# Kernel optimization log

Hardware: AMD Instinct MI355X
Metric: run time of the kernel (lower is better)

## Reference

```python
import jax, jax.numpy as jnp
import numpy as np
import math

EMBED = 512
KDIM = 512
VDIM = 512
H = 8
HD = EMBED // H
N = 2048
L = 2048
B = 4


def setup_inputs() -> dict:
    key = jax.random.key(0)
    ks = jax.random.split(key, 14)
    s = 1.0 / math.sqrt(EMBED)
    return {
        "q": jax.random.normal(ks[0], (N, B, EMBED), jnp.float32),
        "k": jax.random.normal(ks[1], (L, B, KDIM), jnp.float32),
        "v": jax.random.normal(ks[2], (L, B, VDIM), jnp.float32),
        "pe1": jax.random.normal(ks[3], (B, N, 3), jnp.float32),
        "pe2": jax.random.normal(ks[4], (L, 3), jnp.float32),
        "Wq": jax.random.normal(ks[5], (EMBED, EMBED), jnp.float32) * s,
        "bq": jnp.zeros((EMBED,), jnp.float32),
        "Wk": jax.random.normal(ks[6], (EMBED, KDIM), jnp.float32) * s,
        "bk": jnp.zeros((EMBED,), jnp.float32),
        "Wv": jax.random.normal(ks[7], (EMBED, VDIM), jnp.float32) * s,
        "bv": jnp.zeros((EMBED,), jnp.float32),
        "Wo": jax.random.normal(ks[8], (EMBED, EMBED), jnp.float32) * s,
        "bo": jnp.zeros((EMBED,), jnp.float32),
    }


def reference(q, k, v, pe1, pe2, Wq, bq, Wk, bk, Wv, bv, Wo, bo):
    n, b, _ = q.shape
    l = k.shape[0]
    # projections (nn.Linear: x @ W.T + b)
    qp = q @ Wq.T + bq  # (n, b, E)
    kp = k @ Wk.T + bk  # (l, b, E)
    vp = v @ Wv.T + bv  # (l, b, E)
    # split heads -> (b, H, n, hd)
    qh = qp.reshape(n, b, H, HD).transpose(1, 2, 0, 3)
    kh = kp.reshape(l, b, H, HD).transpose(1, 2, 0, 3)
    vh = vp.reshape(l, b, H, HD).transpose(1, 2, 0, 3)
    # relative PE bias: (b, n, l), broadcast over heads
    pe_scores = jnp.einsum('bnc,lc->bnl', pe1, pe2)[:, None, :, :]
    scores = (jnp.einsum('bhnd,bhld->bhnl', qh, kh) + pe_scores) / math.sqrt(HD)
    attn = jax.nn.softmax(scores, axis=-1)
    out = jnp.einsum('bhnl,bhld->bhnd', attn, vh)  # (b, H, n, hd)
    out = out.transpose(2, 0, 1, 3).reshape(n, b, EMBED)
    return out @ Wo.T + bo
```

## Files before the change

kernel.cpp:

```cpp
#include <hip/hip_runtime.h>
#include <math.h>

#define EMBED 512
#define HDIM 64
#define NHEADS 8
#define SEQ_N 2048
#define SEQ_L 2048
#define BATCH 4
#define MROWS (SEQ_N*BATCH)
#define BE (BATCH*EMBED)

#define QSCALE 0.18033688f

typedef _Float16 f16;
typedef _Float16 half8 __attribute__((ext_vector_type(8)));
typedef _Float16 half4 __attribute__((ext_vector_type(4)));
typedef _Float16 half2v __attribute__((ext_vector_type(2)));
typedef float floatx4 __attribute__((ext_vector_type(4)));
typedef float floatx16 __attribute__((ext_vector_type(16)));

static __device__ inline float fast_exp2(float x) {
#if __has_builtin(__builtin_amdgcn_exp2f)
  return __builtin_amdgcn_exp2f(x);
#else
  return __expf(x * 0.69314718056f);
#endif
}

static __device__ inline half2v pk2(float a, float b) {
#if __has_builtin(__builtin_amdgcn_cvt_pkrtz)
  return __builtin_bit_cast(half2v, __builtin_amdgcn_cvt_pkrtz(a, b));
#else
  half2v o; o[0] = (f16)a; o[1] = (f16)b; return o;
#endif
}

static __device__ inline void gload16(const void* g, void* l) {
  __builtin_amdgcn_global_load_lds(
      (__attribute__((address_space(1))) void*)(g),
      (__attribute__((address_space(3))) void*)(l), 16, 0, 0);
}

__global__ __launch_bounds__(256) void cvt_all(const float* __restrict__ q,
                                               const float* __restrict__ k,
                                               const float* __restrict__ v,
                                               const float* __restrict__ Wq,
                                               const float* __restrict__ Wk,
                                               const float* __restrict__ Wv,
                                               const float* __restrict__ Wo,
                                               f16* __restrict__ qb, f16* __restrict__ kb,
                                               f16* __restrict__ vb, f16* __restrict__ Wb) {
  const long TOK = (long)MROWS * EMBED;
  const long WSZ = (long)EMBED * EMBED;
  int y = blockIdx.y;
  long i = ((long)blockIdx.x * 256 + threadIdx.x) * 4;
  if (y < 3) {
    if (i < TOK) {
      const float* s = y == 0 ? q : y == 1 ? k : v;
      f16* d = y == 0 ? qb : y == 1 ? kb : vb;
      float4 f = *reinterpret_cast<const float4*>(s + i);
      half4 o; o[0] = (f16)f.x; o[1] = (f16)f.y; o[2] = (f16)f.z; o[3] = (f16)f.w;
      *reinterpret_cast<half4*>(d + i) = o;
    }
  } else {
    if (i < 4 * WSZ) {
      int sel = (int)(i >> 18);
      long off = i & (WSZ - 1);
      const float* s = sel == 0 ? Wq : sel == 1 ? Wk : sel == 2 ? Wv : Wo;
      float4 f = *reinterpret_cast<const float4*>(s + off);
      half4 o; o[0] = (f16)f.x; o[1] = (f16)f.y; o[2] = (f16)f.z; o[3] = (f16)f.w;
      *reinterpret_cast<half4*>(Wb + i) = o;
    }
  }
}

__global__ __launch_bounds__(256) void gemm_qkv(const f16* __restrict__ A0,
                                                const f16* __restrict__ A1,
                                                const f16* __restrict__ A2,
                                                const f16* __restrict__ W0,
                                                const f16* __restrict__ W1,
                                                const f16* __restrict__ W2,
                                                const float* __restrict__ b0,
                                                const float* __restrict__ b1,
                                                const float* __restrict__ b2,
                                                f16* __restrict__ C0, f16* __restrict__ C1,
                                                f16* __restrict__ C2t) {
  __shared__ alignas(16) unsigned char gsm[34816];
  f16* As = reinterpret_cast<f16*>(gsm);
  f16* Bs = reinterpret_cast<f16*>(gsm + 16384);
  f16* T  = reinterpret_cast<f16*>(gsm);
  const int sel = blockIdx.y >> 2;
  const f16* A = sel == 0 ? A0 : sel == 1 ? A1 : A2;
  const f16* Bt = sel == 0 ? W0 : sel == 1 ? W1 : W2;
  const float* bias = sel == 0 ? b0 : sel == 1 ? b1 : b2;
  const float scl = sel == 0 ? QSCALE : 1.0f;
  const int tid = threadIdx.x;
  const int wave = tid >> 6, lane = tid & 63, quad = lane >> 4, l16 = lane & 15;
  const int wm = wave & 1, wn = wave >> 1;
  const long m0 = (long)blockIdx.x * 128;
  const long n0 = (long)(blockIdx.y & 3) * 128;
  const int srow = lane >> 2;
  const int scol = (lane & 3) * 8;

  const f16* Ag0 = A + (m0 + wave * 32 + srow) * EMBED + scol;
  const f16* Ag1 = A + (m0 + wave * 32 + 16 + srow) * EMBED + scol;
  const f16* Bg0 = Bt + (n0 + wave * 32 + srow) * EMBED + scol;
  const f16* Bg1 = Bt + (n0 + wave * 32 + 16 + srow) * EMBED + scol;

  gload16(Ag0, &As[(wave * 32) * 32]);
  gload16(Ag1, &As[(wave * 32 + 16) * 32]);
  gload16(Bg0, &Bs[(wave * 32) * 32]);
  gload16(Bg1, &Bs[(wave * 32 + 16) * 32]);
  floatx4 acc[4][4] = {};
  asm volatile("s_waitcnt vmcnt(0)" ::: "memory");
  __builtin_amdgcn_s_barrier();

#pragma unroll
  for (int ks = 0; ks < 16; ++ks) {
    const int cur = ks & 1;
    if (ks + 1 < 16) {
      const int k1 = (ks + 1) * 32;
      gload16(Ag0 + k1, &As[(cur ^ 1) * 4096 + (wave * 32) * 32]);
      gload16(Ag1 + k1, &As[(cur ^ 1) * 4096 + (wave * 32 + 16) * 32]);
      gload16(Bg0 + k1, &Bs[(cur ^ 1) * 4096 + (wave * 32) * 32]);
      gload16(Bg1 + k1, &Bs[(cur ^ 1) * 4096 + (wave * 32 + 16) * 32]);
    }
    half8 af[4], bf[4];
#pragma unroll
    for (int i = 0; i < 4; ++i)
      af[i] = *reinterpret_cast<const half8*>(&As[cur * 4096 + (wm * 64 + i * 16 + l16) * 32 + quad * 8]);
#pragma unroll
    for (int j = 0; j < 4; ++j)
      bf[j] = *reinterpret_cast<const half8*>(&Bs[cur * 4096 + (wn * 64 + j * 16 + l16) * 32 + quad * 8]);
#pragma unroll
    for (int i = 0; i < 4; ++i)
#pragma unroll
      for (int j = 0; j < 4; ++j)
        acc[i][j] = __builtin_amdgcn_mfma_f32_16x16x32_f16(af[i], bf[j], acc[i][j], 0, 0, 0);
    if (ks + 1 < 16) {
      asm volatile("s_waitcnt vmcnt(0)" ::: "memory");
      __builtin_amdgcn_s_barrier();
    }
  }

  if (sel != 2) {
    f16* C = sel == 0 ? C0 : C1;
#pragma unroll
    for (int i = 0; i < 4; ++i)
#pragma unroll
      for (int r = 0; r < 4; ++r) {
        long row = m0 + wm * 64 + i * 16 + quad * 4 + r;
#pragma unroll
        for (int j = 0; j < 4; ++j) {
          long col = n0 + wn * 64 + j * 16 + l16;
          float val = (acc[i][j][r] + bias[col]) * scl;
          C[row * EMBED + col] = (f16)val;
        }
      }
  } else {
    __syncthreads();
#pragma unroll
    for (int i = 0; i < 4; ++i)
#pragma unroll
      for (int r = 0; r < 4; ++r) {
        int mrow = wm * 64 + i * 16 + quad * 4 + r;
        int bq = mrow & 3, lt = mrow >> 2;
#pragma unroll
        for (int j = 0; j < 4; ++j) {
          int col = wn * 64 + j * 16 + l16;
          float val = acc[i][j][r] + bias[n0 + col];
          T[col * 136 + bq * 32 + lt] = (f16)val;
        }
      }
    __syncthreads();
    const int h0 = (int)(n0 >> 6);
    const long lbase = m0 >> 2;
#pragma unroll
    for (int it = 0; it < 8; ++it) {
      int f = it * 256 + tid;
      int ls = f & 3, bq = (f >> 2) & 3, d6 = (f >> 4) & 63, hl = f >> 10;
      half8 o = *reinterpret_cast<const half8*>(&T[(hl * 64 + d6) * 136 + bq * 32 + ls * 8]);
      *reinterpret_cast<half8*>(C2t + (((long)bq * 8 + h0 + hl) * 64 + d6) * 2048 + lbase + ls * 8) = o;
    }
  }
}

__global__ __launch_bounds__(256) void gemm_out(const f16* __restrict__ A,
                                                const f16* __restrict__ Bt,
                                                const float* __restrict__ bias,
                                                float* __restrict__ C) {
  __shared__ alignas(16) f16 As[2][128 * 32];
  __shared__ alignas(16) f16 Bs[2][64 * 32];
  const int tid = threadIdx.x;
  const int wave = tid >> 6, lane = tid & 63, quad = lane >> 4, l16 = lane & 15;
  const long m0 = (long)blockIdx.x * 128;
  const long n0 = (long)blockIdx.y * 64;
  const int srow = lane >> 2;
  const int scol = (lane & 3) * 8;

  const f16* Ag0 = A + (m0 + wave * 32 + srow) * EMBED + scol;
  const f16* Ag1 = A + (m0 + wave * 32 + 16 + srow) * EMBED + scol;
  const f16* Bg0 = Bt + (n0 + wave * 16 + srow) * EMBED + scol;

  gload16(Ag0, &As[0][(wave * 32) * 32]);
  gload16(Ag1, &As[0][(wave * 32 + 16) * 32]);
  gload16(Bg0, &Bs[0][(wave * 16) * 32]);
  floatx4 acc[2][4] = {};
  asm volatile("s_waitcnt vmcnt(0)" ::: "memory");
  __builtin_amdgcn_s_barrier();

#pragma unroll
  for (int ks = 0; ks < 16; ++ks) {
    const int cur = ks & 1;
    if (ks + 1 < 16) {
      const int k1 = (ks + 1) * 32;
      gload16(Ag0 + k1, &As[cur ^ 1][(wave * 32) * 32]);
      gload16(Ag1 + k1, &As[cur ^ 1][(wave * 32 + 16) * 32]);
      gload16(Bg0 + k1, &Bs[cur ^ 1][(wave * 16) * 32]);
    }
    half8 af[2], bf[4];
#pragma unroll
    for (int i = 0; i < 2; ++i)
      af[i] = *reinterpret_cast<const half8*>(&As[cur][(wave * 32 + i * 16 + l16) * 32 + quad * 8]);
#pragma unroll
    for (int j = 0; j < 4; ++j)
      bf[j] = *reinterpret_cast<const half8*>(&Bs[cur][(j * 16 + l16) * 32 + quad * 8]);
#pragma unroll
    for (int i = 0; i < 2; ++i)
#pragma unroll
      for (int j = 0; j < 4; ++j)
        acc[i][j] = __builtin_amdgcn_mfma_f32_16x16x32_f16(af[i], bf[j], acc[i][j], 0, 0, 0);
    if (ks + 1 < 16) {
      asm volatile("s_waitcnt vmcnt(0)" ::: "memory");
      __builtin_amdgcn_s_barrier();
    }
  }
#pragma unroll
  for (int i = 0; i < 2; ++i)
#pragma unroll
    for (int r = 0; r < 4; ++r) {
      long row = m0 + wave * 32 + i * 16 + quad * 4 + r;
#pragma unroll
      for (int j = 0; j < 4; ++j) {
        long col = n0 + j * 16 + l16;
        C[row * EMBED + col] = acc[i][j][r] + bias[col];
      }
    }
}

#define KST 88
#define VST 136
#define NCHUNK (SEQ_L / 128)
#define LDSB (128 * KST * 2 + 64 * VST * 2)
__global__ __launch_bounds__(512, 4) void attn_flash(const f16* __restrict__ qp,
                                                     const f16* __restrict__ kp,
                                                     const f16* __restrict__ vt,
                                                     const float* __restrict__ pe1,
                                                     const float* __restrict__ pe2,
                                                     f16* __restrict__ ao) {
  __shared__ alignas(16) unsigned char smem[LDSB];
  f16* Ks = reinterpret_cast<f16*>(smem);
  f16* Vt = reinterpret_cast<f16*>(smem + 128 * KST * 2);
  float* comb = reinterpret_cast<float*>(smem);
  const int tid = threadIdx.x, wave = tid >> 6, lane = tid & 63;
  const int m = lane & 31, h = lane >> 5;
  const int strip = wave & 1;
  const int half = wave >> 1;
  const int n0 = blockIdx.x * 64;
  const int b = blockIdx.y >> 3, hd = blockIdx.y & 7;
  const long headoff = (long)b * EMBED + hd * HDIM;
  const long vhead = (long)blockIdx.y * 64 * 2048;

  {
    int r = tid >> 3, col = (tid & 7) * 8;
    *reinterpret_cast<uint4*>(&Ks[r * KST + col]) =
        *reinterpret_cast<const uint4*>(qp + (long)(n0 + r) * BE + headoff + col);
  }
  for (int c = tid; c < 1024; c += 512) {
    int rv = c >> 4, cv = (c & 15) * 8;
    *reinterpret_cast<uint4*>(&Vt[rv * VST + cv]) =
        *reinterpret_cast<const uint4*>(vt + vhead + (long)rv * 2048 + 0 + cv);
  }
  {
    const uint4 z4 = {0, 0, 0, 0};
    const uint2 z2 = {0, 0};
    int r = tid >> 2, s = tid & 3;
    if (s == 0) *reinterpret_cast<uint2*>(&Ks[r * KST + 68]) = z2;
    else if (s == 1) *reinterpret_cast<uint4*>(&Ks[r * KST + 72]) = z4;
    else if (s == 2) *reinterpret_cast<uint4*>(&Ks[r * KST + 80]) = z4;
  }
  if (tid < 64) {
    long base = ((long)b * SEQ_N + n0 + tid) * 3;
    half4 v8;
    v8[0] = (f16)(pe1[base + 0] * QSCALE);
    v8[1] = (f16)(pe1[base + 1] * QSCALE);
    v8[2] = (f16)(pe1[base + 2] * QSCALE);
    v8[3] = (f16)0.f;
    *reinterpret_cast<half4*>(&Ks[tid * KST + 64]) = v8;
  }
  __syncthreads();

  half8 qf[5];
#pragma unroll
  for (int e = 0; e < 5; ++e)
    qf[e] = *reinterpret_cast<const half8*>(&Ks[(strip * 32 + m) * KST + e * 16 + h * 8]);
  __syncthreads();

  for (int c = tid; c < 1024; c += 512) {
    int r = c >> 3, col = (c & 7) * 8;
    *reinterpret_cast<uint4*>(&Ks[r * KST + col]) =
        *reinterpret_cast<const uint4*>(kp + (long)(0 + r) * BE + headoff + col);
  }
  if (tid < 128) {
    long bb = (long)(0 + tid) * 3;
    half4 p2;
    p2[0] = (f16)pe2[bb + 0]; p2[1] = (f16)pe2[bb + 1];
    p2[2] = (f16)pe2[bb + 2]; p2[3] = (f16)0.f;
    *reinterpret_cast<half4*>(&Ks[tid * KST + 64]) = p2;
  }

  floatx16 oacc[2] = {};
  float lpart = 0.f;

#pragma unroll 1
  for (int c = 0; c < NCHUNK; ++c) {
    __syncthreads();
    {
      const int t = half;
      floatx16 st = {};
#pragma unroll
      for (int e = 0; e < 5; ++e) {
        half8 kf = *reinterpret_cast<const half8*>(&Ks[(t * 32 + m) * KST + e * 16 + h * 8]);
        st = __builtin_amdgcn_mfma_f32_32x32x16_f16(kf, qf[e], st, 0, 0, 0);
      }
      float p[16];
#pragma unroll
      for (int r = 0; r < 16; ++r) {
        p[r] = fast_exp2(st[r]);
        lpart += p[r];
      }
#pragma unroll
      for (int s = 0; s < 4; ++s) {
        half2v u0 = pk2(p[4 * s + 0], p[4 * s + 1]);
        half2v u1 = pk2(p[4 * s + 2], p[4 * s + 3]);
        half4 bp;
        bp[0] = u0[0]; bp[1] = u0[1]; bp[2] = u1[0]; bp[3] = u1[1];
        int lcol = t * 32 + s * 8 + h * 4;
#pragma unroll
        for (int dt = 0; dt < 2; ++dt) {
          half4 vf = *reinterpret_cast<const half4*>(&Vt[(dt * 32 + m) * VST + lcol]);
          oacc[dt] = __builtin_amdgcn_mfma_f32_32x32x8f16(vf, bp, oacc[dt], 0, 0, 0);
        }
      }
    }
    __syncthreads();
    if (c + 1 < NCHUNK) {
      const int l0 = (c + 1) * 128;
      for (int cc = tid; cc < 1024; cc += 512) {
        int r = cc >> 3, col = (cc & 7) * 8;
        *reinterpret_cast<uint4*>(&Ks[r * KST + col]) =
            *reinterpret_cast<const uint4*>(kp + (long)(l0 + r) * BE + headoff + col);
        int rv = cc >> 4, cv = (cc & 15) * 8;
        *reinterpret_cast<uint4*>(&Vt[rv * VST + cv]) =
            *reinterpret_cast<const uint4*>(vt + vhead + (long)rv * 2048 + l0 + cv);
      }
      if (tid < 128) {
        long bb = (long)(l0 + tid) * 3;
        half4 p2;
        p2[0] = (f16)pe2[bb + 0]; p2[1] = (f16)pe2[bb + 1];
        p2[2] = (f16)pe2[bb + 2]; p2[3] = (f16)0.f;
        *reinterpret_cast<half4*>(&Ks[tid * KST + 64]) = p2;
      }
    }
  }

  lpart += __shfl_xor(lpart, 32);

  if (half & 1) {
    float* dst = comb + (((strip << 1) + (half >> 1)) * 64 + lane) * 33;
#pragma unroll
    for (int dt = 0; dt < 2; ++dt)
#pragma unroll
      for (int x = 0; x < 16; ++x) dst[dt * 16 + x] = oacc[dt][x];
    dst[32] = lpart;
  }
  __syncthreads();
  if (!(half & 1)) {
    float* slot = comb + (((strip << 1) + (half >> 1)) * 64 + lane) * 33;
#pragma unroll
    for (int dt = 0; dt < 2; ++dt)
#pragma unroll
      for (int x = 0; x < 16; ++x) oacc[dt][x] += slot[dt * 16 + x];
    lpart += slot[32];
    if (half == 2) {
#pragma unroll
      for (int dt = 0; dt < 2; ++dt)
#pragma unroll
        for (int x = 0; x < 16; ++x) slot[dt * 16 + x] = oacc[dt][x];
      slot[32] = lpart;
    }
  }
  __syncthreads();
  if (half == 0) {
    const float* src = comb + (((strip << 1) + 1) * 64 + lane) * 33;
#pragma unroll
    for (int dt = 0; dt < 2; ++dt)
#pragma unroll
      for (int x = 0; x < 16; ++x) oacc[dt][x] += src[dt * 16 + x];
    float inv = 1.f / (lpart + src[32]);
    long qrow = n0 + strip * 32 + m;
#pragma unroll
    for (int dt = 0; dt < 2; ++dt)
#pragma unroll
      for (int g = 0; g < 4; ++g) {
        half4 o4;
#pragma unroll
        for (int x = 0; x < 4; ++x) o4[x] = (f16)(oacc[dt][4 * g + x] * inv);
        int d = dt * 32 + 8 * g + 4 * h;
        *reinterpret_cast<half4*>(ao + qrow * BE + headoff + d) = o4;
      }
  }
}

extern "C" void kernel_launch(void* const* d_in, const int* in_sizes, int n_in,
                              void* d_out, int out_size, void* d_ws, size_t ws_size,
                              hipStream_t stream) {
  const float* q   = (const float*)d_in[0];
  const float* k   = (const float*)d_in[1];
  const float* v   = (const float*)d_in[2];
  const float* pe1 = (const float*)d_in[3];
  const float* pe2 = (const float*)d_in[4];
  const float* Wq  = (const float*)d_in[5];
  const float* bq  = (const float*)d_in[6];
  const float* Wk  = (const float*)d_in[7];
  const float* bk  = (const float*)d_in[8];
  const float* Wv  = (const float*)d_in[9];
  const float* bv  = (const float*)d_in[10];
  const float* Wo  = (const float*)d_in[11];
  const float* bo  = (const float*)d_in[12];
  float* out = (float*)d_out;

  f16* ws = (f16*)d_ws;
  const long TOK = (long)MROWS * EMBED;
  const long WSZ = (long)EMBED * EMBED;
  f16* qb  = ws;
  f16* kb  = qb + TOK;
  f16* vb  = kb + TOK;
  f16* Wqb = vb + TOK;
  f16* Wkb = Wqb + WSZ;
  f16* Wvb = Wkb + WSZ;
  f16* Wob = Wvb + WSZ;
  f16* qpb = Wob + WSZ;
  f16* kpb = qpb + TOK;
  f16* vtb = kpb + TOK;
  f16* aob = vtb + TOK;

  cvt_all<<<dim3(4096, 4), 256, 0, stream>>>(q, k, v, Wq, Wk, Wv, Wo, qb, kb, vb, Wqb);

  gemm_qkv<<<dim3(MROWS / 128, 12), 256, 0, stream>>>(qb, kb, vb, Wqb, Wkb, Wvb,
                                                      bq, bk, bv, qpb, kpb, vtb);

  attn_flash<<<dim3(SEQ_N / 64, BATCH * NHEADS), 512, 0, stream>>>(qpb, kpb, vtb, pe1, pe2, aob);

  gemm_out<<<dim3(MROWS / 128, EMBED / 64), 256, 0, stream>>>(aob, Wob, bo, out);
}
```

Measured before the change: 213.1 us.

## Double-buffer K/V in attention with async global-to-LDS loads and XOR swizzle

Rewrites the attention kernel's K/V staging. The next chunk is loaded with direct global-to-LDS loads (gload16) into a second buffer while the current chunk is computed, which removes one barrier per iteration. Padded LDS rows are replaced by an XOR-swizzled layout, and the pe2 bias moves into its own small buffer. Each block now covers 128 query rows with 4 strips x 2 halves, so grid size halves and the cross-wave reduction shrinks. The cost is more LDS per block, which may lower occupancy, and fewer blocks in the grid.

```diff
diff --git a/kernel.cpp b/kernel.cpp
--- a/kernel.cpp
+++ b/kernel.cpp
@@ -248,10 +248,11 @@
     }
 }
 
-#define KST 88
-#define VST 136
+#define KBUFB (128 * 64 * 2)
+#define VBUFB (64 * 128 * 2)
+#define PEBUFB (128 * 16 * 2)
+#define LDSB (2 * KBUFB + 2 * VBUFB + 2 * PEBUFB)
 #define NCHUNK (SEQ_L / 128)
-#define LDSB (128 * KST * 2 + 64 * VST * 2)
 __global__ __launch_bounds__(512, 4) void attn_flash(const f16* __restrict__ qp,
                                                      const f16* __restrict__ kp,
                                                      const f16* __restrict__ vt,
@@ -259,79 +260,94 @@
                                                      const float* __restrict__ pe2,
                                                      f16* __restrict__ ao) {
   __shared__ alignas(16) unsigned char smem[LDSB];
-  f16* Ks = reinterpret_cast<f16*>(smem);
-  f16* Vt = reinterpret_cast<f16*>(smem + 128 * KST * 2);
+  f16* K0 = reinterpret_cast<f16*>(smem);
+  f16* V0 = reinterpret_cast<f16*>(smem + 2 * KBUFB);
+  f16* P0 = reinterpret_cast<f16*>(smem + 2 * KBUFB + 2 * VBUFB);
   float* comb = reinterpret_cast<float*>(smem);
   const int tid = threadIdx.x, wave = tid >> 6, lane = tid & 63;
   const int m = lane & 31, h = lane >> 5;
-  const int strip = wave & 1;
-  const int half = wave >> 1;
-  const int n0 = blockIdx.x * 64;
+  const int strip = wave & 3, half = wave >> 2;
+  const int n0 = blockIdx.x * 128;
   const int b = blockIdx.y >> 3, hd = blockIdx.y & 7;
   const long headoff = (long)b * EMBED + hd * HDIM;
   const long vhead = (long)blockIdx.y * 64 * 2048;
 
-  {
-    int r = tid >> 3, col = (tid & 7) * 8;
-    *reinterpret_cast<uint4*>(&Ks[r * KST + col]) =
+  const int krow0 = wave * 16 + (lane >> 3);
+  const int kg = (lane & 7) ^ (lane >> 3);
+  const f16* ksrc0 = kp + headoff + (long)krow0 * BE + kg * 8;
+  const int vd0 = wave * 8 + (lane >> 4);
+  const int vd1 = vd0 + 4;
+  const int vg0 = (lane & 15) ^ (vd0 & 7);
+  const int vg1 = (lane & 15) ^ (vd1 & 7);
+  const f16* vsrc0 = vt + vhead + (long)vd0 * 2048 + vg0 * 8;
+  const f16* vsrc1 = vt + vhead + (long)vd1 * 2048 + vg1 * 8;
+
+  for (int c = tid; c < 1024; c += 512) {
+    int r = c >> 3, col = (c & 7) * 8;
+    *reinterpret_cast<uint4*>(&K0[r * 64 + col]) =
         *reinterpret_cast<const uint4*>(qp + (long)(n0 + r) * BE + headoff + col);
   }
-  for (int c = tid; c < 1024; c += 512) {
-    int rv = c >> 4, cv = (c & 15) * 8;
-    *reinterpret_cast<uint4*>(&Vt[rv * VST + cv]) =
-        *reinterpret_cast<const uint4*>(vt + vhead + (long)rv * 2048 + 0 + cv);
-  }
-  {
+  gload16(vsrc0, V0 + wave * 1024);
+  gload16(vsrc1, V0 + wave * 1024 + 512);
+  if (tid < 256) {
+    const uint2 z2 = {0, 0};
     const uint4 z4 = {0, 0, 0, 0};
-    const uint2 z2 = {0, 0};
-    int r = tid >> 2, s = tid & 3;
-    if (s == 0) *reinterpret_cast<uint2*>(&Ks[r * KST + 68]) = z2;
-    else if (s == 1) *reinterpret_cast<uint4*>(&Ks[r * KST + 72]) = z4;
-    else if (s == 2) *reinterpret_cast<uint4*>(&Ks[r * KST + 80]) = z4;
-  }
-  if (tid < 64) {
+    *reinterpret_cast<uint2*>(reinterpret_cast<char*>(P0) + tid * 32 + 8) = z2;
+    *reinterpret_cast<uint4*>(reinterpret_cast<char*>(P0) + tid * 32 + 16) = z4;
+  }
+  if (tid < 128) {
     long base = ((long)b * SEQ_N + n0 + tid) * 3;
     half4 v8;
     v8[0] = (f16)(pe1[base + 0] * QSCALE);
     v8[1] = (f16)(pe1[base + 1] * QSCALE);
     v8[2] = (f16)(pe1[base + 2] * QSCALE);
     v8[3] = (f16)0.f;
-    *reinterpret_cast<half4*>(&Ks[tid * KST + 64]) = v8;
+    *reinterpret_cast<half4*>(&P0[tid * 16]) = v8;
   }
   __syncthreads();
 
   half8 qf[5];
 #pragma unroll
-  for (int e = 0; e < 5; ++e)
-    qf[e] = *reinterpret_cast<const half8*>(&Ks[(strip * 32 + m) * KST + e * 16 + h * 8]);
+  for (int e = 0; e < 4; ++e)
+    qf[e] = *reinterpret_cast<const half8*>(&K0[(strip * 32 + m) * 64 + e * 16 + h * 8]);
+  qf[4] = *reinterpret_cast<const half8*>(&P0[(strip * 32 + m) * 16 + h * 8]);
   __syncthreads();
 
-  for (int c = tid; c < 1024; c += 512) {
-    int r = c >> 3, col = (c & 7) * 8;
-    *reinterpret_cast<uint4*>(&Ks[r * KST + col]) =
-        *reinterpret_cast<const uint4*>(kp + (long)(0 + r) * BE + headoff + col);
-  }
-  if (tid < 128) {
-    long bb = (long)(0 + tid) * 3;
-    half4 p2;
-    p2[0] = (f16)pe2[bb + 0]; p2[1] = (f16)pe2[bb + 1];
-    p2[2] = (f16)pe2[bb + 2]; p2[3] = (f16)0.f;
-    *reinterpret_cast<half4*>(&Ks[tid * KST + 64]) = p2;
-  }
+  gload16(ksrc0, K0 + wave * 1024);
+  gload16(ksrc0 + 8 * BE, K0 + wave * 1024 + 512);
+  {
+    int pr = tid & 127;
+    float a0 = pe2[(long)pr * 3 + 0];
+    float a1 = pe2[(long)pr * 3 + 1];
+    float a2 = pe2[(long)pr * 3 + 2];
+    if (tid < 128) {
+      half4 p2v; p2v[0] = (f16)a0; p2v[1] = (f16)a1; p2v[2] = (f16)a2; p2v[3] = (f16)0.f;
+      *reinterpret_cast<half4*>(&P0[tid * 16]) = p2v;
+    }
+  }
+  __syncthreads();
 
   floatx16 oacc[2] = {};
   float lpart = 0.f;
 
-#pragma unroll 1
-  for (int c = 0; c < NCHUNK; ++c) {
-    __syncthreads();
-    {
-      const int t = half;
+  auto compute_chunk = [&](int bsel) {
+    const f16* Kb = K0 + bsel * 8192;
+    const f16* Vb = V0 + bsel * 8192;
+    const f16* Pb = P0 + bsel * 2048;
+#pragma unroll
+    for (int tt = 0; tt < 2; ++tt) {
+      const int t = half * 2 + tt;
+      const int row = t * 32 + m;
+      const int r7 = m & 7;
       floatx16 st = {};
 #pragma unroll
-      for (int e = 0; e < 5; ++e) {
-        half8 kf = *reinterpret_cast<const half8*>(&Ks[(t * 32 + m) * KST + e * 16 + h * 8]);
+      for (int e = 0; e < 4; ++e) {
+        half8 kf = *reinterpret_cast<const half8*>(&Kb[row * 64 + (((2 * e + h) ^ r7) * 8)]);
         st = __builtin_amdgcn_mfma_f32_32x32x16_f16(kf, qf[e], st, 0, 0, 0);
+      }
+      {
+        half8 kf = *reinterpret_cast<const half8*>(&Pb[row * 16 + h * 8]);
+        st = __builtin_amdgcn_mfma_f32_32x32x16_f16(kf, qf[4], st, 0, 0, 0);
       }
       float p[16];
 #pragma unroll
@@ -345,39 +361,48 @@
         half2v u1 = pk2(p[4 * s + 2], p[4 * s + 3]);
         half4 bp;
         bp[0] = u0[0]; bp[1] = u0[1]; bp[2] = u1[0]; bp[3] = u1[1];
-        int lcol = t * 32 + s * 8 + h * 4;
+        const int sl = t * 4 + s;
 #pragma unroll
         for (int dt = 0; dt < 2; ++dt) {
-          half4 vf = *reinterpret_cast<const half4*>(&Vt[(dt * 32 + m) * VST + lcol]);
+          const int d = dt * 32 + m;
+          half4 vf = *reinterpret_cast<const half4*>(&Vb[d * 128 + ((sl ^ r7) * 8) + h * 4]);
           oacc[dt] = __builtin_amdgcn_mfma_f32_32x32x8f16(vf, bp, oacc[dt], 0, 0, 0);
         }
       }
     }
+  };
+
+  int buf = 0;
+#pragma unroll 1
+  for (int c = 0; c < NCHUNK - 1; ++c) {
+    const int l0n = (c + 1) * 128;
+    f16* Kn = K0 + (buf ^ 1) * 8192;
+    f16* Vn = V0 + (buf ^ 1) * 8192;
+    gload16(ksrc0 + (long)l0n * BE, Kn + wave * 1024);
+    gload16(ksrc0 + (long)l0n * BE + 8 * BE, Kn + wave * 1024 + 512);
+    gload16(vsrc0 + l0n, Vn + wave * 1024);
+    gload16(vsrc1 + l0n, Vn + wave * 1024 + 512);
+    int pr = tid & 127;
+    float a0 = pe2[(long)(l0n + pr) * 3 + 0];
+    float a1 = pe2[(long)(l0n + pr) * 3 + 1];
+    float a2 = pe2[(long)(l0n + pr) * 3 + 2];
+
+    compute_chunk(buf);
+
+    if (tid < 128) {
+      half4 p2v; p2v[0] = (f16)a0; p2v[1] = (f16)a1; p2v[2] = (f16)a2; p2v[3] = (f16)0.f;
+      *reinterpret_cast<half4*>(&P0[(buf ^ 1) * 2048 + tid * 16]) = p2v;
+    }
     __syncthreads();
-    if (c + 1 < NCHUNK) {
-      const int l0 = (c + 1) * 128;
-      for (int cc = tid; cc < 1024; cc += 512) {
-        int r = cc >> 3, col = (cc & 7) * 8;
-        *reinterpret_cast<uint4*>(&Ks[r * KST + col]) =
-            *reinterpret_cast<const uint4*>(kp + (long)(l0 + r) * BE + headoff + col);
-        int rv = cc >> 4, cv = (cc & 15) * 8;
-        *reinterpret_cast<uint4*>(&Vt[rv * VST + cv]) =
-            *reinterpret_cast<const uint4*>(vt + vhead + (long)rv * 2048 + l0 + cv);
-      }
-      if (tid < 128) {
-        long bb = (long)(l0 + tid) * 3;
-        half4 p2;
-        p2[0] = (f16)pe2[bb + 0]; p2[1] = (f16)pe2[bb + 1];
-        p2[2] = (f16)pe2[bb + 2]; p2[3] = (f16)0.f;
-        *reinterpret_cast<half4*>(&Ks[tid * KST + 64]) = p2;
-      }
-    }
-  }
+    buf ^= 1;
+  }
+  compute_chunk(buf);
+  __syncthreads();
 
   lpart += __shfl_xor(lpart, 32);
 
-  if (half & 1) {
-    float* dst = comb + (((strip << 1) + (half >> 1)) * 64 + lane) * 33;
+  if (half == 1) {
+    float* dst = comb + (strip * 64 + lane) * 33;
 #pragma unroll
     for (int dt = 0; dt < 2; ++dt)
 #pragma unroll
@@ -385,24 +410,8 @@
     dst[32] = lpart;
   }
   __syncthreads();
-  if (!(half & 1)) {
-    float* slot = comb + (((strip << 1) + (half >> 1)) * 64 + lane) * 33;
-#pragma unroll
-    for (int dt = 0; dt < 2; ++dt)
-#pragma unroll
-      for (int x = 0; x < 16; ++x) oacc[dt][x] += slot[dt * 16 + x];
-    lpart += slot[32];
-    if (half == 2) {
-#pragma unroll
-      for (int dt = 0; dt < 2; ++dt)
-#pragma unroll
-        for (int x = 0; x < 16; ++x) slot[dt * 16 + x] = oacc[dt][x];
-      slot[32] = lpart;
-    }
-  }
-  __syncthreads();
   if (half == 0) {
-    const float* src = comb + (((strip << 1) + 1) * 64 + lane) * 33;
+    const float* src = comb + (strip * 64 + lane) * 33;
 #pragma unroll
     for (int dt = 0; dt < 2; ++dt)
 #pragma unroll
@@ -460,7 +469,7 @@
   gemm_qkv<<<dim3(MROWS / 128, 12), 256, 0, stream>>>(qb, kb, vb, Wqb, Wkb, Wvb,
                                                       bq, bk, bv, qpb, kpb, vtb);
 
-  attn_flash<<<dim3(SEQ_N / 64, BATCH * NHEADS), 512, 0, stream>>>(qpb, kpb, vtb, pe1, pe2, aob);
+  attn_flash<<<dim3(SEQ_N / 128, BATCH * NHEADS), 512, 0, stream>>>(qpb, kpb, vtb, pe1, pe2, aob);
 
   gemm_out<<<dim3(MROWS / 128, EMBED / 64), 256, 0, stream>>>(aob, Wob, bo, out);
 }
```

Result: faster. 201.4 us (-5.5%).
